# Optimization experiments

Measured on AMD Instinct MI355X. Metric: run time of the kernel, lower is better.

Reference implementation:

```python
import jax, jax.numpy as jnp
import numpy as np

B, L = 8, 131072
NSEC = 2


def _stable(raw):
    # raw (..., 5) -> stable biquad coeffs [b0,b1,b2,a1,a2]
    b = raw[..., :3]
    a1 = 2.0 * jnp.tanh(raw[..., 3])
    a2 = ((2.0 - jnp.abs(a1)) * jnp.tanh(raw[..., 4]) + jnp.abs(a1)) / 2.0
    return jnp.concatenate([b, a1[..., None], a2[..., None]], axis=-1)


def _biquad(x, c):
    # x: (B, L), c: (B, 5); direct form II transposed IIR
    b0, b1, b2, a1, a2 = (c[:, i] for i in range(5))
    def step(carry, xt):
        s1, s2 = carry
        y = b0 * xt + s1
        s1n = b1 * xt - a1 * y + s2
        s2n = b2 * xt - a2 * y
        return (s1n, s2n), y
    z = jnp.zeros_like(x[:, 0])
    _, ys = jax.lax.scan(step, (z, z), x.T)
    return ys.T


def _envelope(x, coef):
    # one-pole smoother of |x|
    ax = jnp.abs(x)
    def step(e, a):
        en = coef * e + (1.0 - coef) * a
        return en, en
    _, es = jax.lax.scan(step, jnp.zeros_like(x[:, 0]), ax.T)
    return es.T


def _gru(x, wi, wh, bi, bh, ow, ob):
    # torch GRU cell, input_size=1, hidden_size=1, gate order r,z,n
    wi0 = wi[:, 0]
    wh0 = wh[:, 0]
    def step(h, xt):
        gi = xt[:, None] * wi0[None, :] + bi   # (B, 3)
        gh = h[:, None] * wh0[None, :] + bh    # (B, 3)
        r = jax.nn.sigmoid(gi[:, 0] + gh[:, 0])
        z = jax.nn.sigmoid(gi[:, 1] + gh[:, 1])
        n = jnp.tanh(gi[:, 2] + r * gh[:, 2])
        hn = (1.0 - z) * n + z * h
        return hn, hn
    _, hs = jax.lax.scan(step, jnp.zeros_like(x[:, 0]), x.T)
    return hs.T * ow[0] + ob[0]


def setup_inputs() -> dict:
    key = jax.random.key(0)
    ks = jax.random.split(key, 16)
    return {
        "x": 0.3 * jax.random.normal(ks[0], (B, L), dtype=jnp.float32),
        "knobs": jax.random.uniform(ks[1], (B, 3), dtype=jnp.float32),
        "env_coef_raw": jnp.array([3.0], dtype=jnp.float32),  # sigmoid -> ~0.95 smoothing
        "pre_params": 0.3 * jax.random.normal(ks[2], (NSEC, 5), dtype=jnp.float32),
        "post_params": 0.3 * jax.random.normal(ks[3], (NSEC, 5), dtype=jnp.float32),
        "gru_wi": jax.random.normal(ks[4], (3, 1), dtype=jnp.float32),
        "gru_wh": jax.random.normal(ks[5], (3, 1), dtype=jnp.float32),
        "gru_bi": 0.1 * jax.random.normal(ks[6], (3,), dtype=jnp.float32),
        "gru_bh": 0.1 * jax.random.normal(ks[7], (3,), dtype=jnp.float32),
        "gru_ow": jax.random.normal(ks[8], (1,), dtype=jnp.float32),
        "gru_ob": jnp.zeros((1,), dtype=jnp.float32),
        "sag_w1": jax.random.normal(ks[9], (8, 1), dtype=jnp.float32),
        "sag_b1": jnp.zeros((8,), dtype=jnp.float32),
        "sag_w2": jax.random.normal(ks[10], (1, 8), dtype=jnp.float32) / np.sqrt(8.0),
        "sag_b2": jnp.zeros((1,), dtype=jnp.float32),
        "fb_w1": jax.random.normal(ks[11], (16, 2), dtype=jnp.float32),
        "fb_b1": jnp.zeros((16,), dtype=jnp.float32),
        "fb_w2": 0.3 * jax.random.normal(ks[12], (5, 16), dtype=jnp.float32) / np.sqrt(16.0),
        "fb_b2": jnp.zeros((5,), dtype=jnp.float32),
        "fb_amount": jnp.zeros((1,), dtype=jnp.float32),
    }


def reference(x, knobs, env_coef_raw, pre_params, post_params,
              gru_wi, gru_wh, gru_bi, gru_bh, gru_ow, gru_ob,
              sag_w1, sag_b1, sag_w2, sag_b2,
              fb_w1, fb_b1, fb_w2, fb_b2, fb_amount):
    b = x.shape[0]
    sag_knob = knobs[:, 0:1]          # (B, 1)
    fb_knobs = knobs[:, 1:3]          # (B, 2)

    # envelope follower + sag gain modulation
    env = _envelope(x, jax.nn.sigmoid(env_coef_raw[0]))           # (B, L)
    sag_h = jnp.tanh(sag_knob @ sag_w1.T + sag_b1)                # (B, 8)
    sag_depth = jax.nn.sigmoid(sag_h @ sag_w2.T + sag_b2)         # (B, 1)
    y = x * (1.0 - sag_depth * env)

    # pre-filter biquad cascade
    pre = _stable(pre_params)                                     # (NSEC, 5)
    for s in range(NSEC):
        y = _biquad(y, jnp.tile(pre[s][None, :], (b, 1)))

    # GRU nonlinearity
    y = _gru(y, gru_wi, gru_wh, gru_bi, gru_bh, gru_ow, gru_ob)

    # post-filter biquad cascade
    post = _stable(post_params)
    for s in range(NSEC):
        y = _biquad(y, jnp.tile(post[s][None, :], (b, 1)))

    # knob-controlled negative feedback biquad
    fb_h = jnp.tanh(fb_knobs @ fb_w1.T + fb_b1)                   # (B, 16)
    fb_c = _stable(fb_h @ fb_w2.T + fb_b2)                        # (B, 5)
    fb_signal = _biquad(y, fb_c)
    fb_mix = jax.nn.sigmoid(fb_amount[0])
    return y - fb_mix * fb_signal
```

## Files before the change

### kernel.cpp

```cpp
#include <hip/hip_runtime.h>
#include <math.h>

#define NB 8
#define NL 131072

#define CH1 32
#define W1  192
#define CH2 16
#define W2  96
#define W3  128

#define P1 8
#define P2 4
#define P3 8

__device__ float g_buf[NB * NL];

__device__ __forceinline__ float rcp_f(float x) { return __builtin_amdgcn_rcpf(x); }
__device__ __forceinline__ float exp2_f(float x) {
    float r;
    asm("v_exp_f32 %0, %1" : "=v"(r) : "v"(x));
    return r;
}
__device__ __forceinline__ float tanh_mlp(float x) {
    const float s2L = 2.8853900817779268f;
    return fmaf(-2.0f, rcp_f(1.0f + exp2_f(s2L * x)), 1.0f);
}

extern "C" __global__ void __launch_bounds__(64)
k1_pre(const float* __restrict__ x,
       const float* __restrict__ knobs,
       const float* __restrict__ env_coef_raw,
       const float* __restrict__ pre_params,
       const float* __restrict__ sag_w1,
       const float* __restrict__ sag_b1,
       const float* __restrict__ sag_w2,
       const float* __restrict__ sag_b2,
       float* __restrict__ y1)
{
    const int cpr = NL / CH1;
    const int tid = blockIdx.x * blockDim.x + threadIdx.x;
    const int row = tid / cpr;
    const int ch  = tid - row * cpr;

    const float envc = 1.0f / (1.0f + expf(-env_coef_raw[0]));
    const float om_envc = 1.0f - envc;

    const float k0 = knobs[row * 3 + 0];
    float acc = sag_b2[0];
    #pragma unroll
    for (int j = 0; j < 8; ++j) {
        float hj = tanh_mlp(fmaf(k0, sag_w1[j], sag_b1[j]));
        acc = fmaf(hj, sag_w2[j], acc);
    }
    const float d = 1.0f / (1.0f + expf(-acc));

    float b0[2], b1c[2], b2c[2], a1[2], a2[2];
    #pragma unroll
    for (int s = 0; s < 2; ++s) {
        const float* p = pre_params + 5 * s;
        float t1 = 2.0f * tanhf(p[3]);
        float aa = fabsf(t1);
        float t2 = 0.5f * fmaf(2.0f - aa, tanhf(p[4]), aa);
        b0[s] = p[0]; b1c[s] = p[1]; b2c[s] = p[2]; a1[s] = t1; a2[s] = t2;
    }

    float env = 0.0f;
    float s11 = 0.0f, s12 = 0.0f, s21 = 0.0f, s22 = 0.0f;

    const int base = row * NL;
    const int t0   = ch * CH1;
    int tstart = t0 - W1; if (tstart < 0) tstart = 0;
    const int tend = t0 + CH1;
    const int nit  = (tend - tstart) >> 2;

    float4 buf[P1];
    #pragma unroll
    for (int p = 0; p < P1; ++p)
        buf[p] = *(const float4*)(x + base + tstart + 4 * p);

    int t = tstart;
    for (int m = 0; m < nit; m += P1) {
        #pragma unroll
        for (int p = 0; p < P1; ++p) {
            float4 cur = buf[p];
            int tp = t + 4 * P1; if (tp > NL - 4) tp = NL - 4;
            buf[p] = *(const float4*)(x + base + tp);

            float xs[4] = {cur.x, cur.y, cur.z, cur.w};
            float ov[4];
            #pragma unroll
            for (int u = 0; u < 4; ++u) {
                float xt = xs[u];
                float axs = fabsf(xt) * om_envc;
                env = fmaf(envc, env, axs);
                float g = fmaf(-d, env, 1.0f);
                float y = xt * g;
                {
                    float yo = fmaf(b0[0], y, s11);
                    s11 = fmaf(-a1[0], yo, fmaf(b1c[0], y, s12));
                    s12 = fmaf(b2c[0], y, -a2[0] * yo);
                    y = yo;
                }
                {
                    float yo = fmaf(b0[1], y, s21);
                    s21 = fmaf(-a1[1], yo, fmaf(b1c[1], y, s22));
                    s22 = fmaf(b2c[1], y, -a2[1] * yo);
                    y = yo;
                }
                ov[u] = y;
            }
            if (t >= t0)
                *(float4*)(y1 + base + t) = make_float4(ov[0], ov[1], ov[2], ov[3]);
            t += 4;
        }
    }
}

extern "C" __global__ void __launch_bounds__(64)
k2_gru(const float* __restrict__ y1,
       const float* __restrict__ gru_wi,
       const float* __restrict__ gru_wh,
       const float* __restrict__ gru_bi,
       const float* __restrict__ gru_bh)
{
    const int cpr = NL / CH2;
    const int tid = blockIdx.x * blockDim.x + threadIdx.x;
    const int row = tid / cpr;
    const int ch  = tid - row * cpr;

    const float L2E = 1.4426950408889634f;
    const float wi0n = -L2E * gru_wi[0];
    const float wh0n = -L2E * gru_wh[0];
    const float b0n  = -L2E * (gru_bi[0] + gru_bh[0]);
    const float wi1n = -L2E * gru_wi[1];
    const float wh1n = -L2E * gru_wh[1];
    const float b1n  = -L2E * (gru_bi[1] + gru_bh[1]);
    const float s2L  = 2.0f * L2E;
    const float wi2s = s2L * gru_wi[2];
    const float bi2s = s2L * gru_bi[2];
    const float wh2s = s2L * gru_wh[2];
    const float bh2s = s2L * gru_bh[2];

    float h = 0.0f;

    const int base = row * NL;
    const int t0   = ch * CH2;
    int tstart = t0 - W2; if (tstart < 0) tstart = 0;
    const int tend = t0 + CH2;
    const int nit  = (tend - tstart) >> 2;

    float4 buf[P2];
    #pragma unroll
    for (int p = 0; p < P2; ++p)
        buf[p] = *(const float4*)(y1 + base + tstart + 4 * p);

    int t = tstart;
    for (int m = 0; m < nit; m += P2) {
        #pragma unroll
        for (int p = 0; p < P2; ++p) {
            float4 cur = buf[p];
            int tp = t + 4 * P2; if (tp > NL - 4) tp = NL - 4;
            buf[p] = *(const float4*)(y1 + base + tp);

            float ys[4] = {cur.x, cur.y, cur.z, cur.w};
            float ov[4];
            #pragma unroll
            for (int u = 0; u < 4; ++u) {
                float y = ys[u];
                float cr = fmaf(y, wi0n, b0n);
                float cz = fmaf(y, wi1n, b1n);
                float cn = fmaf(y, wi2s, bi2s);
                float wr   = fmaf(h, wh0n, cr);
                float wz   = fmaf(h, wh1n, cz);
                float gh2s = fmaf(h, wh2s, bh2s);
                float Er = exp2_f(wr);
                float Ez = exp2_f(wz);
                float r  = rcp_f(1.0f + Er);
                float v2 = fmaf(r, gh2s, cn);
                float En = exp2_f(v2);
                float num = fmaf(En, Ez + h, h - Ez);
                float den = (En + 1.0f) * (Ez + 1.0f);
                h = num * rcp_f(den);
                ov[u] = h;
            }
            if (t >= t0)
                *(float4*)(g_buf + base + t) = make_float4(ov[0], ov[1], ov[2], ov[3]);
            t += 4;
        }
    }
}

extern "C" __global__ void __launch_bounds__(64)
k3_post(const float* __restrict__ knobs,
        const float* __restrict__ post_params,
        const float* __restrict__ gru_ow,
        const float* __restrict__ gru_ob,
        const float* __restrict__ fb_w1,
        const float* __restrict__ fb_b1,
        const float* __restrict__ fb_w2,
        const float* __restrict__ fb_b2,
        const float* __restrict__ fb_amount,
        float* __restrict__ out)
{
    const int cpr = NL / CH1;
    const int tid = blockIdx.x * blockDim.x + threadIdx.x;
    const int row = tid / cpr;
    const int ch  = tid - row * cpr;

    const float ow = gru_ow[0], ob = gru_ob[0];

    float b0[2], b1c[2], b2c[2], a1[2], a2[2];
    #pragma unroll
    for (int s = 0; s < 2; ++s) {
        const float* p = post_params + 5 * s;
        float t1 = 2.0f * tanhf(p[3]);
        float aa = fabsf(t1);
        float t2 = 0.5f * fmaf(2.0f - aa, tanhf(p[4]), aa);
        b0[s] = p[0]; b1c[s] = p[1]; b2c[s] = p[2]; a1[s] = t1; a2[s] = t2;
    }

    const float k1 = knobs[row * 3 + 1];
    const float k2 = knobs[row * 3 + 2];
    float raw[5];
    #pragma unroll
    for (int i = 0; i < 5; ++i) raw[i] = fb_b2[i];
    #pragma unroll
    for (int j = 0; j < 16; ++j) {
        float hj = tanh_mlp(fmaf(k1, fb_w1[j * 2 + 0], fmaf(k2, fb_w1[j * 2 + 1], fb_b1[j])));
        #pragma unroll
        for (int i = 0; i < 5; ++i) raw[i] = fmaf(hj, fb_w2[i * 16 + j], raw[i]);
    }
    const float fa1 = 2.0f * tanhf(raw[3]);
    const float faa = fabsf(fa1);
    const float fa2 = 0.5f * fmaf(2.0f - faa, tanhf(raw[4]), faa);
    const float fc0 = raw[0], fc1 = raw[1], fc2 = raw[2];
    const float fbmix = 1.0f / (1.0f + expf(-fb_amount[0]));

    float s11 = 0.0f, s12 = 0.0f, s21 = 0.0f, s22 = 0.0f;
    float fs1 = 0.0f, fs2 = 0.0f;

    const int base = row * NL;
    const int t0   = ch * CH1;
    int tstart = t0 - W3; if (tstart < 0) tstart = 0;
    const int tend = t0 + CH1;
    const int nit  = (tend - tstart) >> 2;

    float4 buf[P3];
    #pragma unroll
    for (int p = 0; p < P3; ++p)
        buf[p] = *(const float4*)(g_buf + base + tstart + 4 * p);

    int t = tstart;
    for (int m = 0; m < nit; m += P3) {
        #pragma unroll
        for (int p = 0; p < P3; ++p) {
            float4 cur = buf[p];
            int tp = t + 4 * P3; if (tp > NL - 4) tp = NL - 4;
            buf[p] = *(const float4*)(g_buf + base + tp);

            float hs[4] = {cur.x, cur.y, cur.z, cur.w};
            float ov[4];
            #pragma unroll
            for (int u = 0; u < 4; ++u) {
                float y = fmaf(hs[u], ow, ob);
                {
                    float yo = fmaf(b0[0], y, s11);
                    s11 = fmaf(-a1[0], yo, fmaf(b1c[0], y, s12));
                    s12 = fmaf(b2c[0], y, -a2[0] * yo);
                    y = yo;
                }
                {
                    float yo = fmaf(b0[1], y, s21);
                    s21 = fmaf(-a1[1], yo, fmaf(b1c[1], y, s22));
                    s22 = fmaf(b2c[1], y, -a2[1] * yo);
                    y = yo;
                }
                {
                    float fo = fmaf(fc0, y, fs1);
                    fs1 = fmaf(-fa1, fo, fmaf(fc1, y, fs2));
                    fs2 = fmaf(fc2, y, -fa2 * fo);
                    ov[u] = fmaf(-fbmix, fo, y);
                }
            }
            if (t >= t0)
                *(float4*)(out + base + t) = make_float4(ov[0], ov[1], ov[2], ov[3]);
            t += 4;
        }
    }
}

extern "C" void kernel_launch(void* const* d_in, const int* in_sizes, int n_in,
                              void* d_out, int out_size, void* d_ws, size_t ws_size,
                              hipStream_t stream) {
    const float* x            = (const float*)d_in[0];
    const float* knobs        = (const float*)d_in[1];
    const float* env_coef_raw = (const float*)d_in[2];
    const float* pre_params   = (const float*)d_in[3];
    const float* post_params  = (const float*)d_in[4];
    const float* gru_wi       = (const float*)d_in[5];
    const float* gru_wh       = (const float*)d_in[6];
    const float* gru_bi       = (const float*)d_in[7];
    const float* gru_bh       = (const float*)d_in[8];
    const float* gru_ow       = (const float*)d_in[9];
    const float* gru_ob       = (const float*)d_in[10];
    const float* sag_w1       = (const float*)d_in[11];
    const float* sag_b1       = (const float*)d_in[12];
    const float* sag_w2       = (const float*)d_in[13];
    const float* sag_b2       = (const float*)d_in[14];
    const float* fb_w1        = (const float*)d_in[15];
    const float* fb_b1        = (const float*)d_in[16];
    const float* fb_w2        = (const float*)d_in[17];
    const float* fb_b2        = (const float*)d_in[18];
    const float* fb_amount    = (const float*)d_in[19];
    float* outp = (float*)d_out;

    dim3 block(64);
    dim3 grid13(NB * (NL / CH1) / 64);
    dim3 grid2 (NB * (NL / CH2) / 64);

    k1_pre<<<grid13, block, 0, stream>>>(x, knobs, env_coef_raw, pre_params,
                                         sag_w1, sag_b1, sag_w2, sag_b2, outp);
    k2_gru<<<grid2, block, 0, stream>>>(outp, gru_wi, gru_wh, gru_bi, gru_bh);
    k3_post<<<grid13, block, 0, stream>>>(knobs, post_params, gru_ow, gru_ob,
                                          fb_w1, fb_b1, fb_w2, fb_b2, fb_amount, outp);
}
```

Measured before the change: 130.1 us.

## Fuse three stage kernels into one cooperative kernel with grid syncs

Replaces the three separate launches (pre-filter/envelope, GRU, post-filter/feedback) with one cooperative kernel. The stages are separated by a threadfence and grid.sync, so kernel-boundary and launch overheads go away. All stages now use a common chunk size of 16 with 256-thread blocks and smaller prefetch depths. This doubles the thread count for the pre and post stages and shortens each thread's serial chain. The cost is more redundant warm-up computation, grid-wide barrier latency, and a dependence on all 256 blocks being co-resident.

```diff
diff --git a/kernel.cpp b/kernel.cpp
--- a/kernel.cpp
+++ b/kernel.cpp
@@ -1,18 +1,20 @@
 #include <hip/hip_runtime.h>
+#include <hip/hip_cooperative_groups.h>
 #include <math.h>
+
+namespace cg = cooperative_groups;
 
 #define NB 8
 #define NL 131072
 
-#define CH1 32
+#define CH  16
 #define W1  192
-#define CH2 16
 #define W2  96
 #define W3  128
 
-#define P1 8
-#define P2 4
-#define P3 8
+#define PA 4
+#define PB 4
+#define PC 4
 
 __device__ float g_buf[NB * NL];
 
@@ -27,265 +29,256 @@
     return fmaf(-2.0f, rcp_f(1.0f + exp2_f(s2L * x)), 1.0f);
 }
 
-extern "C" __global__ void __launch_bounds__(64)
-k1_pre(const float* __restrict__ x,
-       const float* __restrict__ knobs,
-       const float* __restrict__ env_coef_raw,
-       const float* __restrict__ pre_params,
-       const float* __restrict__ sag_w1,
-       const float* __restrict__ sag_b1,
-       const float* __restrict__ sag_w2,
-       const float* __restrict__ sag_b2,
-       float* __restrict__ y1)
-{
-    const int cpr = NL / CH1;
-    const int tid = blockIdx.x * blockDim.x + threadIdx.x;
-    const int row = tid / cpr;
-    const int ch  = tid - row * cpr;
-
-    const float envc = 1.0f / (1.0f + expf(-env_coef_raw[0]));
-    const float om_envc = 1.0f - envc;
-
-    const float k0 = knobs[row * 3 + 0];
-    float acc = sag_b2[0];
-    #pragma unroll
-    for (int j = 0; j < 8; ++j) {
-        float hj = tanh_mlp(fmaf(k0, sag_w1[j], sag_b1[j]));
-        acc = fmaf(hj, sag_w2[j], acc);
-    }
-    const float d = 1.0f / (1.0f + expf(-acc));
-
-    float b0[2], b1c[2], b2c[2], a1[2], a2[2];
-    #pragma unroll
-    for (int s = 0; s < 2; ++s) {
-        const float* p = pre_params + 5 * s;
-        float t1 = 2.0f * tanhf(p[3]);
-        float aa = fabsf(t1);
-        float t2 = 0.5f * fmaf(2.0f - aa, tanhf(p[4]), aa);
-        b0[s] = p[0]; b1c[s] = p[1]; b2c[s] = p[2]; a1[s] = t1; a2[s] = t2;
-    }
-
-    float env = 0.0f;
-    float s11 = 0.0f, s12 = 0.0f, s21 = 0.0f, s22 = 0.0f;
-
-    const int base = row * NL;
-    const int t0   = ch * CH1;
-    int tstart = t0 - W1; if (tstart < 0) tstart = 0;
-    const int tend = t0 + CH1;
-    const int nit  = (tend - tstart) >> 2;
-
-    float4 buf[P1];
-    #pragma unroll
-    for (int p = 0; p < P1; ++p)
-        buf[p] = *(const float4*)(x + base + tstart + 4 * p);
-
-    int t = tstart;
-    for (int m = 0; m < nit; m += P1) {
-        #pragma unroll
-        for (int p = 0; p < P1; ++p) {
-            float4 cur = buf[p];
-            int tp = t + 4 * P1; if (tp > NL - 4) tp = NL - 4;
-            buf[p] = *(const float4*)(x + base + tp);
-
-            float xs[4] = {cur.x, cur.y, cur.z, cur.w};
-            float ov[4];
-            #pragma unroll
-            for (int u = 0; u < 4; ++u) {
-                float xt = xs[u];
-                float axs = fabsf(xt) * om_envc;
-                env = fmaf(envc, env, axs);
-                float g = fmaf(-d, env, 1.0f);
-                float y = xt * g;
-                {
-                    float yo = fmaf(b0[0], y, s11);
-                    s11 = fmaf(-a1[0], yo, fmaf(b1c[0], y, s12));
-                    s12 = fmaf(b2c[0], y, -a2[0] * yo);
-                    y = yo;
-                }
-                {
-                    float yo = fmaf(b0[1], y, s21);
-                    s21 = fmaf(-a1[1], yo, fmaf(b1c[1], y, s22));
-                    s22 = fmaf(b2c[1], y, -a2[1] * yo);
-                    y = yo;
-                }
-                ov[u] = y;
-            }
-            if (t >= t0)
-                *(float4*)(y1 + base + t) = make_float4(ov[0], ov[1], ov[2], ov[3]);
-            t += 4;
-        }
-    }
-}
-
-extern "C" __global__ void __launch_bounds__(64)
-k2_gru(const float* __restrict__ y1,
-       const float* __restrict__ gru_wi,
-       const float* __restrict__ gru_wh,
-       const float* __restrict__ gru_bi,
-       const float* __restrict__ gru_bh)
-{
-    const int cpr = NL / CH2;
-    const int tid = blockIdx.x * blockDim.x + threadIdx.x;
-    const int row = tid / cpr;
-    const int ch  = tid - row * cpr;
-
-    const float L2E = 1.4426950408889634f;
-    const float wi0n = -L2E * gru_wi[0];
-    const float wh0n = -L2E * gru_wh[0];
-    const float b0n  = -L2E * (gru_bi[0] + gru_bh[0]);
-    const float wi1n = -L2E * gru_wi[1];
-    const float wh1n = -L2E * gru_wh[1];
-    const float b1n  = -L2E * (gru_bi[1] + gru_bh[1]);
-    const float s2L  = 2.0f * L2E;
-    const float wi2s = s2L * gru_wi[2];
-    const float bi2s = s2L * gru_bi[2];
-    const float wh2s = s2L * gru_wh[2];
-    const float bh2s = s2L * gru_bh[2];
-
-    float h = 0.0f;
-
-    const int base = row * NL;
-    const int t0   = ch * CH2;
-    int tstart = t0 - W2; if (tstart < 0) tstart = 0;
-    const int tend = t0 + CH2;
-    const int nit  = (tend - tstart) >> 2;
-
-    float4 buf[P2];
-    #pragma unroll
-    for (int p = 0; p < P2; ++p)
-        buf[p] = *(const float4*)(y1 + base + tstart + 4 * p);
-
-    int t = tstart;
-    for (int m = 0; m < nit; m += P2) {
-        #pragma unroll
-        for (int p = 0; p < P2; ++p) {
-            float4 cur = buf[p];
-            int tp = t + 4 * P2; if (tp > NL - 4) tp = NL - 4;
-            buf[p] = *(const float4*)(y1 + base + tp);
-
-            float ys[4] = {cur.x, cur.y, cur.z, cur.w};
-            float ov[4];
-            #pragma unroll
-            for (int u = 0; u < 4; ++u) {
-                float y = ys[u];
-                float cr = fmaf(y, wi0n, b0n);
-                float cz = fmaf(y, wi1n, b1n);
-                float cn = fmaf(y, wi2s, bi2s);
-                float wr   = fmaf(h, wh0n, cr);
-                float wz   = fmaf(h, wh1n, cz);
-                float gh2s = fmaf(h, wh2s, bh2s);
-                float Er = exp2_f(wr);
-                float Ez = exp2_f(wz);
-                float r  = rcp_f(1.0f + Er);
-                float v2 = fmaf(r, gh2s, cn);
-                float En = exp2_f(v2);
-                float num = fmaf(En, Ez + h, h - Ez);
-                float den = (En + 1.0f) * (Ez + 1.0f);
-                h = num * rcp_f(den);
-                ov[u] = h;
-            }
-            if (t >= t0)
-                *(float4*)(g_buf + base + t) = make_float4(ov[0], ov[1], ov[2], ov[3]);
-            t += 4;
-        }
-    }
-}
-
-extern "C" __global__ void __launch_bounds__(64)
-k3_post(const float* __restrict__ knobs,
+extern "C" __global__ void __launch_bounds__(256)
+k_fused(const float* __restrict__ x,
+        const float* __restrict__ knobs,
+        const float* __restrict__ env_coef_raw,
+        const float* __restrict__ pre_params,
         const float* __restrict__ post_params,
+        const float* __restrict__ gru_wi,
+        const float* __restrict__ gru_wh,
+        const float* __restrict__ gru_bi,
+        const float* __restrict__ gru_bh,
         const float* __restrict__ gru_ow,
         const float* __restrict__ gru_ob,
+        const float* __restrict__ sag_w1,
+        const float* __restrict__ sag_b1,
+        const float* __restrict__ sag_w2,
+        const float* __restrict__ sag_b2,
         const float* __restrict__ fb_w1,
         const float* __restrict__ fb_b1,
         const float* __restrict__ fb_w2,
         const float* __restrict__ fb_b2,
         const float* __restrict__ fb_amount,
-        float* __restrict__ out)
+        float* __restrict__ outp)
 {
-    const int cpr = NL / CH1;
+    cg::grid_group grid = cg::this_grid();
+
+    const int cpr = NL / CH;
     const int tid = blockIdx.x * blockDim.x + threadIdx.x;
     const int row = tid / cpr;
     const int ch  = tid - row * cpr;
-
-    const float ow = gru_ow[0], ob = gru_ob[0];
-
-    float b0[2], b1c[2], b2c[2], a1[2], a2[2];
-    #pragma unroll
-    for (int s = 0; s < 2; ++s) {
-        const float* p = post_params + 5 * s;
-        float t1 = 2.0f * tanhf(p[3]);
-        float aa = fabsf(t1);
-        float t2 = 0.5f * fmaf(2.0f - aa, tanhf(p[4]), aa);
-        b0[s] = p[0]; b1c[s] = p[1]; b2c[s] = p[2]; a1[s] = t1; a2[s] = t2;
+    const int base = row * NL;
+    const int t0   = ch * CH;
+
+    {
+        const float envc = 1.0f / (1.0f + expf(-env_coef_raw[0]));
+        const float om_envc = 1.0f - envc;
+
+        const float k0 = knobs[row * 3 + 0];
+        float acc = sag_b2[0];
+        #pragma unroll
+        for (int j = 0; j < 8; ++j) {
+            float hj = tanh_mlp(fmaf(k0, sag_w1[j], sag_b1[j]));
+            acc = fmaf(hj, sag_w2[j], acc);
+        }
+        const float d = 1.0f / (1.0f + expf(-acc));
+
+        float b0[2], b1c[2], b2c[2], a1[2], a2[2];
+        #pragma unroll
+        for (int s = 0; s < 2; ++s) {
+            const float* p = pre_params + 5 * s;
+            float t1 = 2.0f * tanhf(p[3]);
+            float aa = fabsf(t1);
+            float t2 = 0.5f * fmaf(2.0f - aa, tanhf(p[4]), aa);
+            b0[s] = p[0]; b1c[s] = p[1]; b2c[s] = p[2]; a1[s] = t1; a2[s] = t2;
+        }
+
+        float env = 0.0f;
+        float s11 = 0.0f, s12 = 0.0f, s21 = 0.0f, s22 = 0.0f;
+
+        int tstart = t0 - W1; if (tstart < 0) tstart = 0;
+        const int tend = t0 + CH;
+        const int nit  = (tend - tstart) >> 2;
+
+        float4 buf[PA];
+        #pragma unroll
+        for (int p = 0; p < PA; ++p)
+            buf[p] = *(const float4*)(x + base + tstart + 4 * p);
+
+        int t = tstart;
+        for (int m = 0; m < nit; m += PA) {
+            #pragma unroll
+            for (int p = 0; p < PA; ++p) {
+                float4 cur = buf[p];
+                int tp = t + 4 * PA; if (tp > NL - 4) tp = NL - 4;
+                buf[p] = *(const float4*)(x + base + tp);
+
+                float xs[4] = {cur.x, cur.y, cur.z, cur.w};
+                float ov[4];
+                #pragma unroll
+                for (int u = 0; u < 4; ++u) {
+                    float xt = xs[u];
+                    float axs = fabsf(xt) * om_envc;
+                    env = fmaf(envc, env, axs);
+                    float g = fmaf(-d, env, 1.0f);
+                    float y = xt * g;
+                    {
+                        float yo = fmaf(b0[0], y, s11);
+                        s11 = fmaf(-a1[0], yo, fmaf(b1c[0], y, s12));
+                        s12 = fmaf(b2c[0], y, -a2[0] * yo);
+                        y = yo;
+                    }
+                    {
+                        float yo = fmaf(b0[1], y, s21);
+                        s21 = fmaf(-a1[1], yo, fmaf(b1c[1], y, s22));
+                        s22 = fmaf(b2c[1], y, -a2[1] * yo);
+                        y = yo;
+                    }
+                    ov[u] = y;
+                }
+                if (t >= t0)
+                    *(float4*)(outp + base + t) = make_float4(ov[0], ov[1], ov[2], ov[3]);
+                t += 4;
+            }
+        }
     }
 
-    const float k1 = knobs[row * 3 + 1];
-    const float k2 = knobs[row * 3 + 2];
-    float raw[5];
-    #pragma unroll
-    for (int i = 0; i < 5; ++i) raw[i] = fb_b2[i];
-    #pragma unroll
-    for (int j = 0; j < 16; ++j) {
-        float hj = tanh_mlp(fmaf(k1, fb_w1[j * 2 + 0], fmaf(k2, fb_w1[j * 2 + 1], fb_b1[j])));
-        #pragma unroll
-        for (int i = 0; i < 5; ++i) raw[i] = fmaf(hj, fb_w2[i * 16 + j], raw[i]);
+    __threadfence();
+    grid.sync();
+
+    {
+        const float L2E = 1.4426950408889634f;
+        const float wi0n = -L2E * gru_wi[0];
+        const float wh0n = -L2E * gru_wh[0];
+        const float b0n  = -L2E * (gru_bi[0] + gru_bh[0]);
+        const float wi1n = -L2E * gru_wi[1];
+        const float wh1n = -L2E * gru_wh[1];
+        const float b1n  = -L2E * (gru_bi[1] + gru_bh[1]);
+        const float s2L  = 2.0f * L2E;
+        const float wi2s = s2L * gru_wi[2];
+        const float bi2s = s2L * gru_bi[2];
+        const float wh2s = s2L * gru_wh[2];
+        const float bh2s = s2L * gru_bh[2];
+
+        float h = 0.0f;
+
+        int tstart = t0 - W2; if (tstart < 0) tstart = 0;
+        const int tend = t0 + CH;
+        const int nit  = (tend - tstart) >> 2;
+
+        float4 buf[PB];
+        #pragma unroll
+        for (int p = 0; p < PB; ++p)
+            buf[p] = *(const float4*)(outp + base + tstart + 4 * p);
+
+        int t = tstart;
+        for (int m = 0; m < nit; m += PB) {
+            #pragma unroll
+            for (int p = 0; p < PB; ++p) {
+                float4 cur = buf[p];
+                int tp = t + 4 * PB; if (tp > NL - 4) tp = NL - 4;
+                buf[p] = *(const float4*)(outp + base + tp);
+
+                float ys[4] = {cur.x, cur.y, cur.z, cur.w};
+                float ov[4];
+                #pragma unroll
+                for (int u = 0; u < 4; ++u) {
+                    float y = ys[u];
+                    float cr = fmaf(y, wi0n, b0n);
+                    float cz = fmaf(y, wi1n, b1n);
+                    float cn = fmaf(y, wi2s, bi2s);
+                    float wr   = fmaf(h, wh0n, cr);
+                    float wz   = fmaf(h, wh1n, cz);
+                    float gh2s = fmaf(h, wh2s, bh2s);
+                    float Er = exp2_f(wr);
+                    float Ez = exp2_f(wz);
+                    float r  = rcp_f(1.0f + Er);
+                    float v2 = fmaf(r, gh2s, cn);
+                    float En = exp2_f(v2);
+                    float num = fmaf(En, Ez + h, h - Ez);
+                    float den = (En + 1.0f) * (Ez + 1.0f);
+                    h = num * rcp_f(den);
+                    ov[u] = h;
+                }
+                if (t >= t0)
+                    *(float4*)(g_buf + base + t) = make_float4(ov[0], ov[1], ov[2], ov[3]);
+                t += 4;
+            }
+        }
     }
-    const float fa1 = 2.0f * tanhf(raw[3]);
-    const float faa = fabsf(fa1);
-    const float fa2 = 0.5f * fmaf(2.0f - faa, tanhf(raw[4]), faa);
-    const float fc0 = raw[0], fc1 = raw[1], fc2 = raw[2];
-    const float fbmix = 1.0f / (1.0f + expf(-fb_amount[0]));
-
-    float s11 = 0.0f, s12 = 0.0f, s21 = 0.0f, s22 = 0.0f;
-    float fs1 = 0.0f, fs2 = 0.0f;
-
-    const int base = row * NL;
-    const int t0   = ch * CH1;
-    int tstart = t0 - W3; if (tstart < 0) tstart = 0;
-    const int tend = t0 + CH1;
-    const int nit  = (tend - tstart) >> 2;
-
-    float4 buf[P3];
-    #pragma unroll
-    for (int p = 0; p < P3; ++p)
-        buf[p] = *(const float4*)(g_buf + base + tstart + 4 * p);
-
-    int t = tstart;
-    for (int m = 0; m < nit; m += P3) {
-        #pragma unroll
-        for (int p = 0; p < P3; ++p) {
-            float4 cur = buf[p];
-            int tp = t + 4 * P3; if (tp > NL - 4) tp = NL - 4;
-            buf[p] = *(const float4*)(g_buf + base + tp);
-
-            float hs[4] = {cur.x, cur.y, cur.z, cur.w};
-            float ov[4];
+
+    __threadfence();
+    grid.sync();
+
+    {
+        const float ow = gru_ow[0], ob = gru_ob[0];
+
+        float b0[2], b1c[2], b2c[2], a1[2], a2[2];
+        #pragma unroll
+        for (int s = 0; s < 2; ++s) {
+            const float* p = post_params + 5 * s;
+            float t1 = 2.0f * tanhf(p[3]);
+            float aa = fabsf(t1);
+            float t2 = 0.5f * fmaf(2.0f - aa, tanhf(p[4]), aa);
+            b0[s] = p[0]; b1c[s] = p[1]; b2c[s] = p[2]; a1[s] = t1; a2[s] = t2;
+        }
+
+        const float k1 = knobs[row * 3 + 1];
+        const float k2 = knobs[row * 3 + 2];
+        float raw[5];
+        #pragma unroll
+        for (int i = 0; i < 5; ++i) raw[i] = fb_b2[i];
+        #pragma unroll
+        for (int j = 0; j < 16; ++j) {
+            float hj = tanh_mlp(fmaf(k1, fb_w1[j * 2 + 0], fmaf(k2, fb_w1[j * 2 + 1], fb_b1[j])));
             #pragma unroll
-            for (int u = 0; u < 4; ++u) {
-                float y = fmaf(hs[u], ow, ob);
-                {
-                    float yo = fmaf(b0[0], y, s11);
-                    s11 = fmaf(-a1[0], yo, fmaf(b1c[0], y, s12));
-                    s12 = fmaf(b2c[0], y, -a2[0] * yo);
-                    y = yo;
+            for (int i = 0; i < 5; ++i) raw[i] = fmaf(hj, fb_w2[i * 16 + j], raw[i]);
+        }
+        const float fa1 = 2.0f * tanhf(raw[3]);
+        const float faa = fabsf(fa1);
+        const float fa2 = 0.5f * fmaf(2.0f - faa, tanhf(raw[4]), faa);
+        const float fc0 = raw[0], fc1 = raw[1], fc2 = raw[2];
+        const float fbmix = 1.0f / (1.0f + expf(-fb_amount[0]));
+
+        float s11 = 0.0f, s12 = 0.0f, s21 = 0.0f, s22 = 0.0f;
+        float fs1 = 0.0f, fs2 = 0.0f;
+
+        int tstart = t0 - W3; if (tstart < 0) tstart = 0;
+        const int tend = t0 + CH;
+        const int nit  = (tend - tstart) >> 2;
+
+        float4 buf[PC];
+        #pragma unroll
+        for (int p = 0; p < PC; ++p)
+            buf[p] = *(const float4*)(g_buf + base + tstart + 4 * p);
+
+        int t = tstart;
+        for (int m = 0; m < nit; m += PC) {
+            #pragma unroll
+            for (int p = 0; p < PC; ++p) {
+                float4 cur = buf[p];
+                int tp = t + 4 * PC; if (tp > NL - 4) tp = NL - 4;
+                buf[p] = *(const float4*)(g_buf + base + tp);
+
+                float hs[4] = {cur.x, cur.y, cur.z, cur.w};
+                float ov[4];
+                #pragma unroll
+                for (int u = 0; u < 4; ++u) {
+                    float y = fmaf(hs[u], ow, ob);
+                    {
+                        float yo = fmaf(b0[0], y, s11);
+                        s11 = fmaf(-a1[0], yo, fmaf(b1c[0], y, s12));
+                        s12 = fmaf(b2c[0], y, -a2[0] * yo);
+                        y = yo;
+                    }
+                    {
+                        float yo = fmaf(b0[1], y, s21);
+                        s21 = fmaf(-a1[1], yo, fmaf(b1c[1], y, s22));
+                        s22 = fmaf(b2c[1], y, -a2[1] * yo);
+                        y = yo;
+                    }
+                    {
+                        float fo = fmaf(fc0, y, fs1);
+                        fs1 = fmaf(-fa1, fo, fmaf(fc1, y, fs2));
+                        fs2 = fmaf(fc2, y, -fa2 * fo);
+                        ov[u] = fmaf(-fbmix, fo, y);
+                    }
                 }
-                {
-                    float yo = fmaf(b0[1], y, s21);
-                    s21 = fmaf(-a1[1], yo, fmaf(b1c[1], y, s22));
-                    s22 = fmaf(b2c[1], y, -a2[1] * yo);
-                    y = yo;
-                }
-                {
-                    float fo = fmaf(fc0, y, fs1);
-                    fs1 = fmaf(-fa1, fo, fmaf(fc1, y, fs2));
-                    fs2 = fmaf(fc2, y, -fa2 * fo);
-                    ov[u] = fmaf(-fbmix, fo, y);
-                }
+                if (t >= t0)
+                    *(float4*)(outp + base + t) = make_float4(ov[0], ov[1], ov[2], ov[3]);
+                t += 4;
             }
-            if (t >= t0)
-                *(float4*)(out + base + t) = make_float4(ov[0], ov[1], ov[2], ov[3]);
-            t += 4;
         }
     }
 }
@@ -315,13 +308,16 @@
     const float* fb_amount    = (const float*)d_in[19];
     float* outp = (float*)d_out;
 
-    dim3 block(64);
-    dim3 grid13(NB * (NL / CH1) / 64);
-    dim3 grid2 (NB * (NL / CH2) / 64);
-
-    k1_pre<<<grid13, block, 0, stream>>>(x, knobs, env_coef_raw, pre_params,
-                                         sag_w1, sag_b1, sag_w2, sag_b2, outp);
-    k2_gru<<<grid2, block, 0, stream>>>(outp, gru_wi, gru_wh, gru_bi, gru_bh);
-    k3_post<<<grid13, block, 0, stream>>>(knobs, post_params, gru_ow, gru_ob,
-                                          fb_w1, fb_b1, fb_w2, fb_b2, fb_amount, outp);
+    void* args[] = {
+        (void*)&x, (void*)&knobs, (void*)&env_coef_raw, (void*)&pre_params,
+        (void*)&post_params, (void*)&gru_wi, (void*)&gru_wh, (void*)&gru_bi,
+        (void*)&gru_bh, (void*)&gru_ow, (void*)&gru_ob, (void*)&sag_w1,
+        (void*)&sag_b1, (void*)&sag_w2, (void*)&sag_b2, (void*)&fb_w1,
+        (void*)&fb_b1, (void*)&fb_w2, (void*)&fb_b2, (void*)&fb_amount,
+        (void*)&outp
+    };
+
+    dim3 grid(NB * (NL / CH) / 256);
+    dim3 block(256);
+    hipLaunchCooperativeKernel((void*)k_fused, grid, block, args, 0, stream);
 }
```

Result: slower. 268.7 us (+106.5%).
